# Optimization experiments

Hardware: AMD Instinct MI355X
Metric: run time of the kernel (lower is better)

## Reference

```python
import jax, jax.numpy as jnp
import numpy as np

N_NODES = 50000
N_EDGES = 800000
IN_CH = 128
HID = 64
HEADS = 4
OUT_CH = 10
NUM_GRAPHS = 500
NEG_SLOPE = 0.2  # PyG GATConv default LeakyReLU slope


def gat_conv(x, src, dst, W, a_src, a_dst, b, concat):
    """One PyG-style GATConv (inference; attention dropout disabled).
    x: [N, F_in], src/dst: [E'] (self-loops already appended).
    W: [F_in, H*C], a_src/a_dst: [H, C], b: [H*C] or [C].
    """
    N = x.shape[0]
    H, C = a_src.shape
    h = (x @ W).reshape(N, H, C)                      # [N,H,C]
    al_s = jnp.einsum('nhc,hc->nh', h, a_src)          # [N,H]
    al_d = jnp.einsum('nhc,hc->nh', h, a_dst)          # [N,H]
    e = al_s[src] + al_d[dst]                          # [E,H]
    e = jnp.where(e > 0, e, NEG_SLOPE * e)             # leaky_relu
    # segment softmax over edges sharing the same destination node
    e_max = jax.ops.segment_max(e, dst, num_segments=N)
    ex = jnp.exp(e - e_max[dst])
    denom = jax.ops.segment_sum(ex, dst, num_segments=N)
    alpha = ex / (denom[dst] + 1e-16)                  # [E,H]
    msg = h[src] * alpha[:, :, None]                   # [E,H,C]
    out = jax.ops.segment_sum(msg, dst, num_segments=N)  # [N,H,C]
    out = out.reshape(N, H * C) if concat else out.mean(axis=1)
    return out + b


def _forward(x, edge_index, batch, W1, a_src1, a_dst1, b1,
             W2, a_src2, a_dst2, b2, fc_w, fc_b):
    N = x.shape[0]
    loops = jnp.arange(N, dtype=edge_index.dtype)
    src = jnp.concatenate([edge_index[0], loops])
    dst = jnp.concatenate([edge_index[1], loops])
    h = gat_conv(x, src, dst, W1, a_src1, a_dst1, b1, concat=True)
    h = jax.nn.relu(h)                                  # dropout: eval mode
    h = gat_conv(h, src, dst, W2, a_src2, a_dst2, b2, concat=False)
    pooled = jax.ops.segment_sum(h, batch, num_segments=NUM_GRAPHS)  # global_add_pool
    logits = pooled @ fc_w + fc_b
    return jax.nn.log_softmax(logits, axis=1)


def setup_inputs() -> dict:
    key = jax.random.key(0)
    ks = jax.random.split(key, 12)
    g = lambda k, shp, fan: jax.random.normal(k, shp, dtype=jnp.float32) * (1.0 / np.sqrt(fan))
    x = jax.random.normal(ks[0], (N_NODES, IN_CH), dtype=jnp.float32)
    edge_index = jax.random.randint(ks[1], (2, N_EDGES), 0, N_NODES, dtype=jnp.int64)
    batch = jnp.sort(jax.random.randint(ks[2], (N_NODES,), 0, NUM_GRAPHS, dtype=jnp.int64))
    return {
        'x': x,
        'edge_index': edge_index,
        'batch': batch,
        'W1': g(ks[3], (IN_CH, HEADS * HID), IN_CH),
        'a_src1': g(ks[4], (HEADS, HID), HID),
        'a_dst1': g(ks[5], (HEADS, HID), HID),
        'b1': jnp.zeros((HEADS * HID,), dtype=jnp.float32),
        'W2': g(ks[6], (HEADS * HID, HID), HEADS * HID),
        'a_src2': g(ks[7], (1, HID), HID),
        'a_dst2': g(ks[8], (1, HID), HID),
        'b2': jnp.zeros((HID,), dtype=jnp.float32),
        'fc_w': g(ks[9], (HID, OUT_CH), HID),
        'fc_b': jnp.zeros((OUT_CH,), dtype=jnp.float32),
    }


def reference(x, edge_index, batch, W1, a_src1, a_dst1, b1,
              W2, a_src2, a_dst2, b2, fc_w, fc_b):
    return _forward(x, edge_index, batch, W1, a_src1, a_dst1, b1,
                    W2, a_src2, a_dst2, b2, fc_w, fc_b)
```

## Files before the change

kernel.cpp:

```cpp
#include <hip/hip_runtime.h>
#include <hip/hip_bf16.h>
#include <math.h>

#define N_NODES   50000
#define N_EDGES   800000
#define EP        (N_EDGES + N_NODES)
#define IN_CH     128
#define HID       64
#define HEADS     4
#define F1        (HEADS * HID)
#define OUT_CH    10
#define NUM_GRAPHS 500
#define NEG_SLOPE 0.2f
#define RPAD      132
#define NTILES    (N_NODES / 16)
#define SCAT_B    ((EP + 255) / 256)
#define CAP       64

typedef __attribute__((ext_vector_type(8))) short short8;
typedef __attribute__((ext_vector_type(4))) float floatx4;

__device__ __forceinline__ unsigned short f2bf(float f) {
    unsigned int u = __float_as_uint(f);
    u += 0x7FFFu + ((u >> 16) & 1u);
    return (unsigned short)(u >> 16);
}
__device__ __forceinline__ unsigned int pack_bf2(float lo, float hi) {
    return (unsigned int)f2bf(lo) | ((unsigned int)f2bf(hi) << 16);
}
__device__ __forceinline__ float bf_lo(unsigned int u) { return __uint_as_float(u << 16); }
__device__ __forceinline__ float bf_hi(unsigned int u) { return __uint_as_float(u & 0xFFFF0000u); }
__device__ __forceinline__ float bf1(unsigned short h) { return __uint_as_float(((unsigned int)h) << 16); }

__global__ void init_kernel(int* __restrict__ cnt,
                            const float* __restrict__ W1, unsigned short* __restrict__ W1p,
                            const float* __restrict__ W2, unsigned short* __restrict__ W2p)
{
    const int gid = blockIdx.x * blockDim.x + threadIdx.x;
    if (gid < N_NODES) cnt[gid] = 0;
    if (gid < 4096) {
        const int t = gid >> 8, kt = (gid >> 6) & 3, l = gid & 63;
        const int col = t * 16 + (l & 15);
        unsigned short* o = W1p + (size_t)((t * 4 + kt) * 64 + l) * 8;
        #pragma unroll
        for (int j = 0; j < 8; ++j) {
            const int k = kt * 32 + (l >> 4) * 8 + j;
            o[j] = f2bf(W1[k * F1 + col]);
        }
    } else if (gid < 6144) {
        const int g2 = gid - 4096;
        const int t = g2 >> 9, kt = (g2 >> 6) & 7, l = g2 & 63;
        const int col = t * 16 + (l & 15);
        unsigned short* o = W2p + (size_t)((t * 8 + kt) * 64 + l) * 8;
        #pragma unroll
        for (int j = 0; j < 8; ++j) {
            const int k = kt * 32 + (l >> 4) * 8 + j;
            o[j] = f2bf(W2[k * HID + col]);
        }
    }
}

__global__ __launch_bounds__(256) void scatter_gemm1(
    const int* __restrict__ ei, int* __restrict__ cnt,
    unsigned short* __restrict__ csr,
    const float* __restrict__ x, const short* __restrict__ W1p,
    const float* __restrict__ a_src1, const float* __restrict__ a_dst1,
    unsigned short* __restrict__ H1b,
    float* __restrict__ al_s1, float* __restrict__ al_d1)
{
    const int e = blockIdx.x * 256 + threadIdx.x;
    if (e < EP) {
        int src, dst;
        if (e < N_EDGES) { src = ei[e]; dst = ei[N_EDGES + e]; }
        else             { src = dst = e - N_EDGES; }
        const int slot = atomicAdd(&cnt[dst], 1);
        if (slot < CAP) csr[dst * CAP + slot] = (unsigned short)src;
    }
    if (blockIdx.x >= NTILES) return;

    const int m0 = blockIdx.x * 16;
    const int w = threadIdx.x >> 6;
    const int l = threadIdx.x & 63;
    const int q = l >> 4, r = l & 15;
    floatx4 acc[4] = {};
    const float* arow = x + (size_t)(m0 + r) * IN_CH + q * 8;
    #pragma unroll
    for (int kt = 0; kt < 4; ++kt) {
        const float4 f0 = *(const float4*)(arow + kt * 32);
        const float4 f1 = *(const float4*)(arow + kt * 32 + 4);
        union { uint4 u; short8 s; } a;
        a.u = make_uint4(pack_bf2(f0.x, f0.y), pack_bf2(f0.z, f0.w),
                         pack_bf2(f1.x, f1.y), pack_bf2(f1.z, f1.w));
        #pragma unroll
        for (int t = 0; t < 4; ++t) {
            const int nt = w * 4 + t;
            const short8 b = *(const short8*)(W1p + (size_t)((nt * 4 + kt) * 64 + l) * 8);
            acc[t] = __builtin_amdgcn_mfma_f32_16x16x32_bf16(a.s, b, acc[t], 0, 0, 0);
        }
    }
    float ls[4] = {0.f, 0.f, 0.f, 0.f}, ld[4] = {0.f, 0.f, 0.f, 0.f};
    #pragma unroll
    for (int t = 0; t < 4; ++t) {
        const int col = (w * 4 + t) * 16 + r;
        const float as = a_src1[col], ad = a_dst1[col];
        #pragma unroll
        for (int reg = 0; reg < 4; ++reg) {
            H1b[(size_t)(m0 + q * 4 + reg) * F1 + col] = f2bf(acc[t][reg]);
            ls[reg] += acc[t][reg] * as;
            ld[reg] += acc[t][reg] * ad;
        }
    }
    #pragma unroll
    for (int reg = 0; reg < 4; ++reg) {
        #pragma unroll
        for (int off = 8; off > 0; off >>= 1) {
            ls[reg] += __shfl_down(ls[reg], off, 16);
            ld[reg] += __shfl_down(ld[reg], off, 16);
        }
    }
    if (r == 0) {
        #pragma unroll
        for (int reg = 0; reg < 4; ++reg) {
            const int n = m0 + q * 4 + reg;
            al_s1[n * HEADS + w] = ls[reg];
            al_d1[n * HEADS + w] = ld[reg];
        }
    }
}

__global__ __launch_bounds__(256) void agg1_gemm2(
    const int* __restrict__ cnt, const unsigned short* __restrict__ csr,
    const float* __restrict__ al_s1, const float* __restrict__ al_d1,
    const uint2* __restrict__ H1b2, const float* __restrict__ b1,
    const short* __restrict__ W2p,
    const float* __restrict__ a_src2, const float* __restrict__ a_dst2,
    unsigned short* __restrict__ H2b,
    float* __restrict__ al_s2, float* __restrict__ al_d2)
{
    const int m0 = blockIdx.x * 16;
    const int w = threadIdx.x >> 6;
    const int l = threadIdx.x & 63;
    __shared__ unsigned int rows[16][RPAD];

    const int h = l >> 4;
    for (int d = 0; d < 4; ++d) {
        const int dst = m0 + w * 4 + d;
        const int n = min(cnt[dst], CAP);
        const float4 ad = *(const float4*)(al_d1 + dst * 4);
        float a0 = 0.f, a1 = 0.f, a2 = 0.f, a3 = 0.f, den = 0.f;
        int s_reg = 0;
        float w0 = 0.f, w1 = 0.f, w2 = 0.f, w3 = 0.f;
        if (l < n) {
            s_reg = csr[dst * CAP + l];
            const float4 as = *(const float4*)(al_s1 + s_reg * 4);
            float t0 = as.x + ad.x; t0 = t0 > 0.f ? t0 : NEG_SLOPE * t0;
            float t1 = as.y + ad.y; t1 = t1 > 0.f ? t1 : NEG_SLOPE * t1;
            float t2 = as.z + ad.z; t2 = t2 > 0.f ? t2 : NEG_SLOPE * t2;
            float t3 = as.w + ad.w; t3 = t3 > 0.f ? t3 : NEG_SLOPE * t3;
            w0 = __expf(t0); w1 = __expf(t1); w2 = __expf(t2); w3 = __expf(t3);
        }
        const int n4 = (n + 3) & ~3;
        for (int i = 0; i < n4; i += 4) {
            int   srcj[4];
            float wtj[4];
            #pragma unroll
            for (int j = 0; j < 4; ++j) {
                const int idx = i + j;
                srcj[j] = __shfl(s_reg, idx, 64);
                const float t0 = __shfl(w0, idx, 64);
                const float t1 = __shfl(w1, idx, 64);
                const float t2 = __shfl(w2, idx, 64);
                const float t3 = __shfl(w3, idx, 64);
                wtj[j] = h == 0 ? t0 : (h == 1 ? t1 : (h == 2 ? t2 : t3));
            }
            uint2 u[4];
            #pragma unroll
            for (int j = 0; j < 4; ++j)
                u[j] = H1b2[(size_t)srcj[j] * (F1 / 4) + l];
            #pragma unroll
            for (int j = 0; j < 4; ++j) {
                a0 += wtj[j] * bf_lo(u[j].x); a1 += wtj[j] * bf_hi(u[j].x);
                a2 += wtj[j] * bf_lo(u[j].y); a3 += wtj[j] * bf_hi(u[j].y);
                den += wtj[j];
            }
        }
        const float rcp = 1.f / (den + 1e-16f);
        const float4 bb = *(const float4*)(b1 + 4 * l);
        float v0 = a0 * rcp + bb.x; v0 = v0 > 0.f ? v0 : 0.f;
        float v1 = a1 * rcp + bb.y; v1 = v1 > 0.f ? v1 : 0.f;
        float v2 = a2 * rcp + bb.z; v2 = v2 > 0.f ? v2 : 0.f;
        float v3 = a3 * rcp + bb.w; v3 = v3 > 0.f ? v3 : 0.f;
        rows[w * 4 + d][2 * l]     = pack_bf2(v0, v1);
        rows[w * 4 + d][2 * l + 1] = pack_bf2(v2, v3);
    }
    __syncthreads();

    const int q = l >> 4, r = l & 15;
    floatx4 acc = {};
    #pragma unroll
    for (int kt = 0; kt < 8; ++kt) {
        union { uint4 u; short8 s; } a;
        a.u = *(const uint4*)&rows[r][kt * 16 + q * 4];
        const short8 b = *(const short8*)(W2p + (size_t)((w * 8 + kt) * 64 + l) * 8);
        acc = __builtin_amdgcn_mfma_f32_16x16x32_bf16(a.s, b, acc, 0, 0, 0);
    }
    const int col = w * 16 + r;
    const float as = a_src2[col], ad2 = a_dst2[col];
    float ls[4], ld[4];
    #pragma unroll
    for (int reg = 0; reg < 4; ++reg) {
        H2b[(size_t)(m0 + q * 4 + reg) * HID + col] = f2bf(acc[reg]);
        ls[reg] = acc[reg] * as;
        ld[reg] = acc[reg] * ad2;
    }
    #pragma unroll
    for (int reg = 0; reg < 4; ++reg) {
        #pragma unroll
        for (int off = 8; off > 0; off >>= 1) {
            ls[reg] += __shfl_down(ls[reg], off, 16);
            ld[reg] += __shfl_down(ld[reg], off, 16);
        }
    }
    __shared__ float Ls[4][16], Ld[4][16];
    if (r == 0) {
        #pragma unroll
        for (int reg = 0; reg < 4; ++reg) {
            Ls[w][q * 4 + reg] = ls[reg];
            Ld[w][q * 4 + reg] = ld[reg];
        }
    }
    __syncthreads();
    if (threadIdx.x < 16) {
        const int row = threadIdx.x;
        al_s2[m0 + row] = Ls[0][row] + Ls[1][row] + Ls[2][row] + Ls[3][row];
        al_d2[m0 + row] = Ld[0][row] + Ld[1][row] + Ld[2][row] + Ld[3][row];
    }
}

__global__ __launch_bounds__(256) void agg2_csr(
    const int* __restrict__ cnt, const unsigned short* __restrict__ csr,
    const float* __restrict__ al_s2, const float* __restrict__ al_d2,
    const uint2* __restrict__ H2b2, uint2* __restrict__ out2b)
{
    const int dst = blockIdx.x * 4 + (threadIdx.x >> 6);
    const int l = threadIdx.x & 63;
    const int qt = l >> 4, j = l & 15;
    const int n = min(cnt[dst], CAP);
    const float ad = al_d2[dst];
    float a0 = 0.f, a1 = 0.f, a2 = 0.f, a3 = 0.f, den = 0.f;
    int s_reg = 0;
    float w_reg = 0.f;
    if (l < n) {
        s_reg = csr[dst * CAP + l];
        float t = al_s2[s_reg] + ad;
        t = t > 0.f ? t : NEG_SLOPE * t;
        w_reg = __expf(t);
    }
    const int n8 = (n + 7) & ~7;
    for (int i = 0; i < n8; i += 8) {
        const int e0 = i + qt, e1 = i + 4 + qt;
        const int   src0 = __shfl(s_reg, e0, 64), src1 = __shfl(s_reg, e1, 64);
        const float wt0  = __shfl(w_reg, e0, 64), wt1  = __shfl(w_reg, e1, 64);
        const uint2 u0 = H2b2[(size_t)src0 * (HID / 4) + j];
        const uint2 u1 = H2b2[(size_t)src1 * (HID / 4) + j];
        a0 += wt0 * bf_lo(u0.x) + wt1 * bf_lo(u1.x);
        a1 += wt0 * bf_hi(u0.x) + wt1 * bf_hi(u1.x);
        a2 += wt0 * bf_lo(u0.y) + wt1 * bf_lo(u1.y);
        a3 += wt0 * bf_hi(u0.y) + wt1 * bf_hi(u1.y);
        den += wt0 + wt1;
    }
    #pragma unroll
    for (int m = 16; m <= 32; m <<= 1) {
        a0 += __shfl_xor(a0, m, 64);
        a1 += __shfl_xor(a1, m, 64);
        a2 += __shfl_xor(a2, m, 64);
        a3 += __shfl_xor(a3, m, 64);
        den += __shfl_xor(den, m, 64);
    }
    if (l < 16) {
        const float rcp = 1.f / (den + 1e-16f);
        out2b[(size_t)dst * (HID / 4) + j] =
            make_uint2(pack_bf2(a0 * rcp, a1 * rcp), pack_bf2(a2 * rcp, a3 * rcp));
    }
}

__global__ __launch_bounds__(256) void pool_fc_kernel(
    const unsigned short* __restrict__ out2b, const float* __restrict__ b2,
    const int* __restrict__ batch,
    const float* __restrict__ fc_w, const float* __restrict__ fc_b,
    float* __restrict__ out)
{
    const int g = blockIdx.x;
    const int q = threadIdx.x >> 6, c = threadIdx.x & 63;
    __shared__ int se[2];
    __shared__ float partial[4][HID];
    __shared__ float pl[HID];
    __shared__ float logits[OUT_CH];
    if (threadIdx.x < 2) {
        const int target = g + threadIdx.x;
        int lo = 0, hi = N_NODES;
        while (lo < hi) { int mid = (lo + hi) >> 1; if (batch[mid] < target) lo = mid + 1; else hi = mid; }
        se[threadIdx.x] = lo;
    }
    __syncthreads();
    const int start = se[0], end = se[1];
    float acc = 0.f;
    for (int n = start + q; n < end; n += 4)
        acc += bf1(out2b[(size_t)n * HID + c]);
    partial[q][c] = acc;
    __syncthreads();
    if (q == 0)
        pl[c] = partial[0][c] + partial[1][c] + partial[2][c] + partial[3][c]
              + (float)(end - start) * b2[c];
    __syncthreads();
    if (threadIdx.x < OUT_CH) {
        float l = fc_b[threadIdx.x];
        #pragma unroll
        for (int k = 0; k < HID; ++k) l += pl[k] * fc_w[k * OUT_CH + threadIdx.x];
        logits[threadIdx.x] = l;
    }
    __syncthreads();
    if (threadIdx.x == 0) {
        float m = logits[0];
        #pragma unroll
        for (int j2 = 1; j2 < OUT_CH; ++j2) m = fmaxf(m, logits[j2]);
        float s = 0.f;
        #pragma unroll
        for (int j2 = 0; j2 < OUT_CH; ++j2) s += __expf(logits[j2] - m);
        const float lse = m + __logf(s);
        #pragma unroll
        for (int j2 = 0; j2 < OUT_CH; ++j2) out[g * OUT_CH + j2] = logits[j2] - lse;
    }
}


extern "C" void kernel_launch(void* const* d_in, const int* in_sizes, int n_in,
                              void* d_out, int out_size, void* d_ws, size_t ws_size,
                              hipStream_t stream)
{
    const float* x      = (const float*)d_in[0];
    const int*   ei     = (const int*)  d_in[1];
    const int*   batch  = (const int*)  d_in[2];
    const float* W1     = (const float*)d_in[3];
    const float* a_src1 = (const float*)d_in[4];
    const float* a_dst1 = (const float*)d_in[5];
    const float* b1     = (const float*)d_in[6];
    const float* W2     = (const float*)d_in[7];
    const float* a_src2 = (const float*)d_in[8];
    const float* a_dst2 = (const float*)d_in[9];
    const float* b2     = (const float*)d_in[10];
    const float* fc_w   = (const float*)d_in[11];
    const float* fc_b   = (const float*)d_in[12];
    float* out = (float*)d_out;

    char* ws = (char*)d_ws;
    size_t off = 0;
    auto alloc_b = [&](size_t bytes) { void* p = (void*)(ws + off); off += (bytes + 15) & ~15ull; return p; };

    unsigned short* H1b  = (unsigned short*)alloc_b((size_t)N_NODES * F1 * 2);
    float* al_s1  = (float*)alloc_b((size_t)N_NODES * HEADS * 4);
    float* al_d1  = (float*)alloc_b((size_t)N_NODES * HEADS * 4);
    unsigned short* H2b  = (unsigned short*)alloc_b((size_t)N_NODES * HID * 2);
    float* al_s2  = (float*)alloc_b((size_t)N_NODES * 4);
    float* al_d2  = (float*)alloc_b((size_t)N_NODES * 4);
    unsigned short* out2b = (unsigned short*)alloc_b((size_t)N_NODES * HID * 2);
    int*   cnt    = (int*)alloc_b((size_t)N_NODES * 4);
    unsigned short* csr = (unsigned short*)alloc_b((size_t)N_NODES * CAP * 2);
    unsigned short* W1p = (unsigned short*)alloc_b((size_t)IN_CH * F1 * 2);
    unsigned short* W2p = (unsigned short*)alloc_b((size_t)F1 * HID * 2);

    init_kernel<<<(N_NODES + 255) / 256, 256, 0, stream>>>(cnt, W1, W1p, W2, W2p);

    scatter_gemm1<<<SCAT_B, 256, 0, stream>>>(ei, cnt, csr, x, (const short*)W1p,
                                              a_src1, a_dst1, H1b, al_s1, al_d1);

    agg1_gemm2<<<N_NODES / 16, 256, 0, stream>>>(cnt, csr, al_s1, al_d1,
                                                 (const uint2*)H1b, b1,
                                                 (const short*)W2p, a_src2, a_dst2,
                                                 H2b, al_s2, al_d2);

    agg2_csr<<<N_NODES / 4, 256, 0, stream>>>(cnt, csr, al_s2, al_d2,
                                              (const uint2*)H2b, (uint2*)out2b);

    pool_fc_kernel<<<NUM_GRAPHS, 256, 0, stream>>>(out2b, b2, batch, fc_w, fc_b, out);
}
```

Baseline: 249.7 us.

## Overlap CSR atomics with GEMM1, stage attention weights in LDS, switch to fp16

The scatter kernel now launches exactly one block per GEMM tile, since the edge count divides evenly into those blocks. Each thread issues its edge's atomic slot reservation first and writes the CSR entry only after the MFMA work, so the atomic latency can overlap the GEMM. Self-loops are written during init instead of being scattered with the other edges. In agg1, the per-edge source offsets and exp weights are staged in shared memory, replacing the per-iteration wave shuffles, and gathers use precomputed byte offsets. All bf16 storage and MFMA is switched to fp16, which trades dynamic range for mantissa precision and adds a risk of overflow on large activations.

New measurement: 240.0 us. -3.9%, faster.

```diff
diff --git a/kernel.cpp b/kernel.cpp
--- a/kernel.cpp
+++ b/kernel.cpp
@@ -1,10 +1,9 @@
 #include <hip/hip_runtime.h>
-#include <hip/hip_bf16.h>
+#include <hip/hip_fp16.h>
 #include <math.h>
 
 #define N_NODES   50000
 #define N_EDGES   800000
-#define EP        (N_EDGES + N_NODES)
 #define IN_CH     128
 #define HID       64
 #define HEADS     4
@@ -14,30 +13,32 @@
 #define NEG_SLOPE 0.2f
 #define RPAD      132
 #define NTILES    (N_NODES / 16)
-#define SCAT_B    ((EP + 255) / 256)
 #define CAP       64
 
-typedef __attribute__((ext_vector_type(8))) short short8;
+typedef __attribute__((ext_vector_type(8))) _Float16 half8;
 typedef __attribute__((ext_vector_type(4))) float floatx4;
 
-__device__ __forceinline__ unsigned short f2bf(float f) {
-    unsigned int u = __float_as_uint(f);
-    u += 0x7FFFu + ((u >> 16) & 1u);
-    return (unsigned short)(u >> 16);
-}
-__device__ __forceinline__ unsigned int pack_bf2(float lo, float hi) {
-    return (unsigned int)f2bf(lo) | ((unsigned int)f2bf(hi) << 16);
-}
-__device__ __forceinline__ float bf_lo(unsigned int u) { return __uint_as_float(u << 16); }
-__device__ __forceinline__ float bf_hi(unsigned int u) { return __uint_as_float(u & 0xFFFF0000u); }
-__device__ __forceinline__ float bf1(unsigned short h) { return __uint_as_float(((unsigned int)h) << 16); }
-
-__global__ void init_kernel(int* __restrict__ cnt,
+__device__ __forceinline__ unsigned short f2h(float f) {
+    _Float16 h = (_Float16)f;
+    unsigned short u; __builtin_memcpy(&u, &h, 2); return u;
+}
+__device__ __forceinline__ unsigned int pack_h2(float lo, float hi) {
+    auto r = __builtin_amdgcn_cvt_pkrtz(lo, hi);
+    unsigned int u; __builtin_memcpy(&u, &r, 4); return u;
+}
+__device__ __forceinline__ float h2f(unsigned short u) {
+    _Float16 h; __builtin_memcpy(&h, &u, 2); return (float)h;
+}
+
+__global__ void init_kernel(int* __restrict__ cnt, unsigned short* __restrict__ csr,
                             const float* __restrict__ W1, unsigned short* __restrict__ W1p,
                             const float* __restrict__ W2, unsigned short* __restrict__ W2p)
 {
     const int gid = blockIdx.x * blockDim.x + threadIdx.x;
-    if (gid < N_NODES) cnt[gid] = 0;
+    if (gid < N_NODES) {
+        cnt[gid] = 1;
+        csr[gid * CAP] = (unsigned short)gid;
+    }
     if (gid < 4096) {
         const int t = gid >> 8, kt = (gid >> 6) & 3, l = gid & 63;
         const int col = t * 16 + (l & 15);
@@ -45,7 +46,7 @@
         #pragma unroll
         for (int j = 0; j < 8; ++j) {
             const int k = kt * 32 + (l >> 4) * 8 + j;
-            o[j] = f2bf(W1[k * F1 + col]);
+            o[j] = f2h(W1[k * F1 + col]);
         }
     } else if (gid < 6144) {
         const int g2 = gid - 4096;
@@ -55,7 +56,7 @@
         #pragma unroll
         for (int j = 0; j < 8; ++j) {
             const int k = kt * 32 + (l >> 4) * 8 + j;
-            o[j] = f2bf(W2[k * HID + col]);
+            o[j] = f2h(W2[k * HID + col]);
         }
     }
 }
@@ -63,20 +64,15 @@
 __global__ __launch_bounds__(256) void scatter_gemm1(
     const int* __restrict__ ei, int* __restrict__ cnt,
     unsigned short* __restrict__ csr,
-    const float* __restrict__ x, const short* __restrict__ W1p,
+    const float* __restrict__ x, const unsigned short* __restrict__ W1p,
     const float* __restrict__ a_src1, const float* __restrict__ a_dst1,
     unsigned short* __restrict__ H1b,
     float* __restrict__ al_s1, float* __restrict__ al_d1)
 {
     const int e = blockIdx.x * 256 + threadIdx.x;
-    if (e < EP) {
-        int src, dst;
-        if (e < N_EDGES) { src = ei[e]; dst = ei[N_EDGES + e]; }
-        else             { src = dst = e - N_EDGES; }
-        const int slot = atomicAdd(&cnt[dst], 1);
-        if (slot < CAP) csr[dst * CAP + slot] = (unsigned short)src;
-    }
-    if (blockIdx.x >= NTILES) return;
+    const int src = ei[e];
+    const int dst = ei[N_EDGES + e];
+    const int slot = atomicAdd(&cnt[dst], 1);
 
     const int m0 = blockIdx.x * 16;
     const int w = threadIdx.x >> 6;
@@ -88,14 +84,14 @@
     for (int kt = 0; kt < 4; ++kt) {
         const float4 f0 = *(const float4*)(arow + kt * 32);
         const float4 f1 = *(const float4*)(arow + kt * 32 + 4);
-        union { uint4 u; short8 s; } a;
-        a.u = make_uint4(pack_bf2(f0.x, f0.y), pack_bf2(f0.z, f0.w),
-                         pack_bf2(f1.x, f1.y), pack_bf2(f1.z, f1.w));
+        union { uint4 u; half8 h; } a;
+        a.u = make_uint4(pack_h2(f0.x, f0.y), pack_h2(f0.z, f0.w),
+                         pack_h2(f1.x, f1.y), pack_h2(f1.z, f1.w));
         #pragma unroll
         for (int t = 0; t < 4; ++t) {
             const int nt = w * 4 + t;
-            const short8 b = *(const short8*)(W1p + (size_t)((nt * 4 + kt) * 64 + l) * 8);
-            acc[t] = __builtin_amdgcn_mfma_f32_16x16x32_bf16(a.s, b, acc[t], 0, 0, 0);
+            const half8 b = *(const half8*)(W1p + (size_t)((nt * 4 + kt) * 64 + l) * 8);
+            acc[t] = __builtin_amdgcn_mfma_f32_16x16x32_f16(a.h, b, acc[t], 0, 0, 0);
         }
     }
     float ls[4] = {0.f, 0.f, 0.f, 0.f}, ld[4] = {0.f, 0.f, 0.f, 0.f};
@@ -105,7 +101,7 @@
         const float as = a_src1[col], ad = a_dst1[col];
         #pragma unroll
         for (int reg = 0; reg < 4; ++reg) {
-            H1b[(size_t)(m0 + q * 4 + reg) * F1 + col] = f2bf(acc[t][reg]);
+            H1b[(size_t)(m0 + q * 4 + reg) * F1 + col] = f2h(acc[t][reg]);
             ls[reg] += acc[t][reg] * as;
             ld[reg] += acc[t][reg] * ad;
         }
@@ -126,13 +122,15 @@
             al_d1[n * HEADS + w] = ld[reg];
         }
     }
+
+    if (slot < CAP) csr[dst * CAP + slot] = (unsigned short)src;
 }
 
 __global__ __launch_bounds__(256) void agg1_gemm2(
     const int* __restrict__ cnt, const unsigned short* __restrict__ csr,
     const float* __restrict__ al_s1, const float* __restrict__ al_d1,
     const uint2* __restrict__ H1b2, const float* __restrict__ b1,
-    const short* __restrict__ W2p,
+    const unsigned short* __restrict__ W2p,
     const float* __restrict__ a_src2, const float* __restrict__ a_dst2,
     unsigned short* __restrict__ H2b,
     float* __restrict__ al_s2, float* __restrict__ al_d2)
@@ -141,47 +139,61 @@
     const int w = threadIdx.x >> 6;
     const int l = threadIdx.x & 63;
     __shared__ unsigned int rows[16][RPAD];
-
-    const int h = l >> 4;
+    __shared__ unsigned int sofs[16][CAP];
+    __shared__ float        wts[16][CAP][4];
+
+    int nreg[4];
+    #pragma unroll
     for (int d = 0; d < 4; ++d) {
-        const int dst = m0 + w * 4 + d;
-        const int n = min(cnt[dst], CAP);
-        const float4 ad = *(const float4*)(al_d1 + dst * 4);
-        float a0 = 0.f, a1 = 0.f, a2 = 0.f, a3 = 0.f, den = 0.f;
-        int s_reg = 0;
+        const int dd = w * 4 + d;
+        const int dstn = m0 + dd;
+        const int n = min(cnt[dstn], CAP);
+        nreg[d] = n;
+        const float4 ad = *(const float4*)(al_d1 + dstn * 4);
         float w0 = 0.f, w1 = 0.f, w2 = 0.f, w3 = 0.f;
+        unsigned int off = 0;
         if (l < n) {
-            s_reg = csr[dst * CAP + l];
-            const float4 as = *(const float4*)(al_s1 + s_reg * 4);
+            const int s = csr[dstn * CAP + l];
+            off = (unsigned int)s << 9;
+            const float4 as = *(const float4*)(al_s1 + s * 4);
             float t0 = as.x + ad.x; t0 = t0 > 0.f ? t0 : NEG_SLOPE * t0;
             float t1 = as.y + ad.y; t1 = t1 > 0.f ? t1 : NEG_SLOPE * t1;
             float t2 = as.z + ad.z; t2 = t2 > 0.f ? t2 : NEG_SLOPE * t2;
             float t3 = as.w + ad.w; t3 = t3 > 0.f ? t3 : NEG_SLOPE * t3;
             w0 = __expf(t0); w1 = __expf(t1); w2 = __expf(t2); w3 = __expf(t3);
         }
+        sofs[dd][l] = off;
+        *(float4*)wts[dd][l] = make_float4(w0, w1, w2, w3);
+    }
+    __syncthreads();
+
+    const int h = l >> 4;
+    const unsigned int lane8 = (unsigned int)(l * 8);
+    #pragma unroll 1
+    for (int d = 0; d < 4; ++d) {
+        const int dd = w * 4 + d;
+        const int n = nreg[d];
+        float a0 = 0.f, a1 = 0.f, a2 = 0.f, a3 = 0.f, den = 0.f;
         const int n4 = (n + 3) & ~3;
         for (int i = 0; i < n4; i += 4) {
-            int   srcj[4];
-            float wtj[4];
+            unsigned int off[4]; float wt[4];
             #pragma unroll
             for (int j = 0; j < 4; ++j) {
-                const int idx = i + j;
-                srcj[j] = __shfl(s_reg, idx, 64);
-                const float t0 = __shfl(w0, idx, 64);
-                const float t1 = __shfl(w1, idx, 64);
-                const float t2 = __shfl(w2, idx, 64);
-                const float t3 = __shfl(w3, idx, 64);
-                wtj[j] = h == 0 ? t0 : (h == 1 ? t1 : (h == 2 ? t2 : t3));
+                off[j] = sofs[dd][i + j];
+                wt[j]  = wts[dd][i + j][h];
             }
             uint2 u[4];
             #pragma unroll
             for (int j = 0; j < 4; ++j)
-                u[j] = H1b2[(size_t)srcj[j] * (F1 / 4) + l];
+                u[j] = *(const uint2*)((const char*)H1b2 + (off[j] + lane8));
             #pragma unroll
             for (int j = 0; j < 4; ++j) {
-                a0 += wtj[j] * bf_lo(u[j].x); a1 += wtj[j] * bf_hi(u[j].x);
-                a2 += wtj[j] * bf_lo(u[j].y); a3 += wtj[j] * bf_hi(u[j].y);
-                den += wtj[j];
+                union { uint2 v; _Float16 hv[4]; } c; c.v = u[j];
+                a0 += wt[j] * (float)c.hv[0];
+                a1 += wt[j] * (float)c.hv[1];
+                a2 += wt[j] * (float)c.hv[2];
+                a3 += wt[j] * (float)c.hv[3];
+                den += wt[j];
             }
         }
         const float rcp = 1.f / (den + 1e-16f);
@@ -190,8 +202,7 @@
         float v1 = a1 * rcp + bb.y; v1 = v1 > 0.f ? v1 : 0.f;
         float v2 = a2 * rcp + bb.z; v2 = v2 > 0.f ? v2 : 0.f;
         float v3 = a3 * rcp + bb.w; v3 = v3 > 0.f ? v3 : 0.f;
-        rows[w * 4 + d][2 * l]     = pack_bf2(v0, v1);
-        rows[w * 4 + d][2 * l + 1] = pack_bf2(v2, v3);
+        *(uint2*)&rows[dd][2 * l] = make_uint2(pack_h2(v0, v1), pack_h2(v2, v3));
     }
     __syncthreads();
 
@@ -199,17 +210,17 @@
     floatx4 acc = {};
     #pragma unroll
     for (int kt = 0; kt < 8; ++kt) {
-        union { uint4 u; short8 s; } a;
+        union { uint4 u; half8 hh; } a;
         a.u = *(const uint4*)&rows[r][kt * 16 + q * 4];
-        const short8 b = *(const short8*)(W2p + (size_t)((w * 8 + kt) * 64 + l) * 8);
-        acc = __builtin_amdgcn_mfma_f32_16x16x32_bf16(a.s, b, acc, 0, 0, 0);
+        const half8 b = *(const half8*)(W2p + (size_t)((w * 8 + kt) * 64 + l) * 8);
+        acc = __builtin_amdgcn_mfma_f32_16x16x32_f16(a.hh, b, acc, 0, 0, 0);
     }
     const int col = w * 16 + r;
     const float as = a_src2[col], ad2 = a_dst2[col];
     float ls[4], ld[4];
     #pragma unroll
     for (int reg = 0; reg < 4; ++reg) {
-        H2b[(size_t)(m0 + q * 4 + reg) * HID + col] = f2bf(acc[reg]);
+        H2b[(size_t)(m0 + q * 4 + reg) * HID + col] = f2h(acc[reg]);
         ls[reg] = acc[reg] * as;
         ld[reg] = acc[reg] * ad2;
     }
@@ -263,10 +274,11 @@
         const float wt0  = __shfl(w_reg, e0, 64), wt1  = __shfl(w_reg, e1, 64);
         const uint2 u0 = H2b2[(size_t)src0 * (HID / 4) + j];
         const uint2 u1 = H2b2[(size_t)src1 * (HID / 4) + j];
-        a0 += wt0 * bf_lo(u0.x) + wt1 * bf_lo(u1.x);
-        a1 += wt0 * bf_hi(u0.x) + wt1 * bf_hi(u1.x);
-        a2 += wt0 * bf_lo(u0.y) + wt1 * bf_lo(u1.y);
-        a3 += wt0 * bf_hi(u0.y) + wt1 * bf_hi(u1.y);
+        union { uint2 v; _Float16 hv[4]; } c0, c1; c0.v = u0; c1.v = u1;
+        a0 += wt0 * (float)c0.hv[0] + wt1 * (float)c1.hv[0];
+        a1 += wt0 * (float)c0.hv[1] + wt1 * (float)c1.hv[1];
+        a2 += wt0 * (float)c0.hv[2] + wt1 * (float)c1.hv[2];
+        a3 += wt0 * (float)c0.hv[3] + wt1 * (float)c1.hv[3];
         den += wt0 + wt1;
     }
     #pragma unroll
@@ -280,7 +292,7 @@
     if (l < 16) {
         const float rcp = 1.f / (den + 1e-16f);
         out2b[(size_t)dst * (HID / 4) + j] =
-            make_uint2(pack_bf2(a0 * rcp, a1 * rcp), pack_bf2(a2 * rcp, a3 * rcp));
+            make_uint2(pack_h2(a0 * rcp, a1 * rcp), pack_h2(a2 * rcp, a3 * rcp));
     }
 }
 
@@ -306,7 +318,7 @@
     const int start = se[0], end = se[1];
     float acc = 0.f;
     for (int n = start + q; n < end; n += 4)
-        acc += bf1(out2b[(size_t)n * HID + c]);
+        acc += h2f(out2b[(size_t)n * HID + c]);
     partial[q][c] = acc;
     __syncthreads();
     if (q == 0)
@@ -314,10 +326,10 @@
               + (float)(end - start) * b2[c];
     __syncthreads();
     if (threadIdx.x < OUT_CH) {
-        float l = fc_b[threadIdx.x];
-        #pragma unroll
-        for (int k = 0; k < HID; ++k) l += pl[k] * fc_w[k * OUT_CH + threadIdx.x];
-        logits[threadIdx.x] = l;
+        float lg = fc_b[threadIdx.x];
+        #pragma unroll
+        for (int k = 0; k < HID; ++k) lg += pl[k] * fc_w[k * OUT_CH + threadIdx.x];
+        logits[threadIdx.x] = lg;
     }
     __syncthreads();
     if (threadIdx.x == 0) {
@@ -369,14 +381,14 @@
     unsigned short* W1p = (unsigned short*)alloc_b((size_t)IN_CH * F1 * 2);
     unsigned short* W2p = (unsigned short*)alloc_b((size_t)F1 * HID * 2);
 
-    init_kernel<<<(N_NODES + 255) / 256, 256, 0, stream>>>(cnt, W1, W1p, W2, W2p);
-
-    scatter_gemm1<<<SCAT_B, 256, 0, stream>>>(ei, cnt, csr, x, (const short*)W1p,
+    init_kernel<<<(N_NODES + 255) / 256, 256, 0, stream>>>(cnt, csr, W1, W1p, W2, W2p);
+
+    scatter_gemm1<<<NTILES, 256, 0, stream>>>(ei, cnt, csr, x, W1p,
                                               a_src1, a_dst1, H1b, al_s1, al_d1);
 
     agg1_gemm2<<<N_NODES / 16, 256, 0, stream>>>(cnt, csr, al_s1, al_d1,
                                                  (const uint2*)H1b, b1,
-                                                 (const short*)W2p, a_src2, a_dst2,
+                                                 W2p, a_src2, a_dst2,
                                                  H2b, al_s2, al_d2);
 
     agg2_csr<<<N_NODES / 4, 256, 0, stream>>>(cnt, csr, al_s2, al_d2,
```
